# Performance work log

Hardware: AMD Instinct MI355X
Metric: run time of the kernel (lower is better)

## Reference

```python
import jax, jax.numpy as jnp
import numpy as np

L, B, T, C, H, V = 12, 4, 1024, 768, 12, 50257
D = C // H
SCALE = 1.0 / float(np.sqrt(D))
EPS = 1e-5


def layernorm(x, g, b):
    m = jnp.mean(x, axis=-1, keepdims=True)
    v = jnp.var(x, axis=-1, keepdims=True)
    return (x - m) / jnp.sqrt(v + EPS) * g + b


def setup_inputs() -> dict:
    key = jax.random.key(0)
    ks = jax.random.split(key, 12)
    w = lambda k, shape: jax.random.normal(k, shape, jnp.float32) * 0.02
    return {
        "idx": jax.random.randint(ks[0], (B, T), 0, V),
        "tok_emb": w(ks[1], (V, C)),
        "pos_emb": w(ks[2], (1, T, C)),
        # per-layer stacked params (leading dim L); Linear stored [in, out]
        "wq": w(ks[3], (L, C, C)), "bq": jnp.zeros((L, C)),
        "wk": w(ks[4], (L, C, C)), "bk": jnp.zeros((L, C)),
        "wv": w(ks[5], (L, C, C)), "bv": jnp.zeros((L, C)),
        "wo": w(ks[6], (L, C, C)), "bo": jnp.zeros((L, C)),
        "ln1_g": jnp.ones((L, C)), "ln1_b": jnp.zeros((L, C)),
        "ln2_g": jnp.ones((L, C)), "ln2_b": jnp.zeros((L, C)),
        "w1": w(ks[7], (L, C, 4 * C)), "b1": jnp.zeros((L, 4 * C)),
        "w2": w(ks[8], (L, 4 * C, C)), "b2": jnp.zeros((L, C)),
        "lnf_g": jnp.ones((C,)), "lnf_b": jnp.zeros((C,)),
        "head_w": w(ks[9], (C, V)),
    }


def gpt_forward(idx, tok_emb, pos_emb, wq, bq, wk, bk, wv, bv, wo, bo,
                ln1_g, ln1_b, ln2_g, ln2_b, w1, b1, w2, b2,
                lnf_g, lnf_b, head_w):
    t = idx.shape[1]
    x = tok_emb[idx] + pos_emb[:, :t, :]                     # [B,T,C]
    mask = jnp.tril(jnp.ones((t, t), dtype=bool))            # causal

    def block(x, p):
        (pwq, pbq, pwk, pbk, pwv, pbv, pwo, pbo,
         g1, be1, g2, be2, pw1, pb1, pw2, pb2) = p
        h = layernorm(x, g1, be1)
        q = (h @ pwq + pbq).reshape(B, t, H, D)
        k = (h @ pwk + pbk).reshape(B, t, H, D)
        v = (h @ pwv + pbv).reshape(B, t, H, D)
        att = jnp.einsum('bthd,bshd->bhts', q, k) * SCALE    # [B,H,T,T]
        att = jnp.where(mask, att, -jnp.inf)
        att = jax.nn.softmax(att, axis=-1)
        y = jnp.einsum('bhts,bshd->bthd', att, v).reshape(B, t, C)
        x = x + y @ pwo + pbo
        h = layernorm(x, g2, be2)
        x = x + jax.nn.gelu(h @ pw1 + pb1, approximate=False) @ pw2 + pb2
        return x, None

    x, _ = jax.lax.scan(block, x, (wq, bq, wk, bk, wv, bv, wo, bo,
                                   ln1_g, ln1_b, ln2_g, ln2_b,
                                   w1, b1, w2, b2))
    x = layernorm(x, lnf_g, lnf_b)
    return x @ head_w                                        # logits [B,T,V]


def reference(idx, tok_emb, pos_emb, wq, bq, wk, bk, wv, bv, wo, bo,
              ln1_g, ln1_b, ln2_g, ln2_b, w1, b1, w2, b2,
              lnf_g, lnf_b, head_w):
    return gpt_forward(idx, tok_emb, pos_emb, wq, bq, wk, bk, wv, bv, wo, bo,
                       ln1_g, ln1_b, ln2_g, ln2_b, w1, b1, w2, b2,
                       lnf_g, lnf_b, head_w)
```

## Files before the change

### kernel.cpp

```cpp
#include <hip/hip_runtime.h>
#include <hip/hip_bf16.h>
#include <math.h>

#define L_ 12
#define B_ 4
#define T_ 1024
#define C_ 768
#define H_ 12
#define D_ 64
#define V_ 50257
#define M_ 4096
#define QKVN 2304
#define FF_ 3072
#define VPAD_ 50432

typedef __hip_bfloat16 bf16;
typedef __attribute__((ext_vector_type(4))) float f32x4;
typedef __attribute__((ext_vector_type(8))) short short8;
typedef __attribute__((ext_vector_type(8))) __bf16 bf16x8;

typedef __attribute__((address_space(1))) void gvoid;
typedef __attribute__((address_space(3))) void svoid;

__device__ __forceinline__ f32x4 mfma_bf16(short8 a, short8 b, f32x4 c) {
  return __builtin_amdgcn_mfma_f32_16x16x32_bf16(
      __builtin_bit_cast(bf16x8, a), __builtin_bit_cast(bf16x8, b), c, 0, 0, 0);
}

__device__ __forceinline__ void gload_lds16(const void* g, void* l) {
  __builtin_amdgcn_global_load_lds((gvoid*)(void*)g, (svoid*)l, 16, 0, 0);
}

__device__ __forceinline__ short f2bf(float x) {
  return __builtin_bit_cast(short, __float2bfloat16(x));
}

__global__ __launch_bounds__(256) void embed_kernel(const int* __restrict__ idx,
    const float* __restrict__ tok, const float* __restrict__ pos, float* __restrict__ x)
{
  const int row = blockIdx.x;
  const int t = row & (T_ - 1);
  const int id = idx[row];
  const float* te = tok + (size_t)id * C_;
  const float* pe = pos + (size_t)t * C_;
  float* xr = x + (size_t)row * C_;
  const int tid = threadIdx.x;
  xr[tid]       = te[tid]       + pe[tid];
  xr[tid + 256] = te[tid + 256] + pe[tid + 256];
  xr[tid + 512] = te[tid + 512] + pe[tid + 512];
}

__global__ __launch_bounds__(256) void ln_kernel(const float* __restrict__ x,
    const float* __restrict__ g, const float* __restrict__ be, bf16* __restrict__ out)
{
  const int row = blockIdx.x;
  const int tid = threadIdx.x;
  const float* xr = x + (size_t)row * C_;
  float v0 = xr[tid], v1 = xr[tid + 256], v2 = xr[tid + 512];
  float s = v0 + v1 + v2;
  float ss = v0 * v0 + v1 * v1 + v2 * v2;
#pragma unroll
  for (int o = 32; o >= 1; o >>= 1) { s += __shfl_xor(s, o, 64); ss += __shfl_xor(ss, o, 64); }
  __shared__ float sm[8];
  const int w = tid >> 6;
  if ((tid & 63) == 0) { sm[w] = s; sm[4 + w] = ss; }
  __syncthreads();
  s = sm[0] + sm[1] + sm[2] + sm[3];
  ss = sm[4] + sm[5] + sm[6] + sm[7];
  const float mean = s * (1.0f / C_);
  const float var = ss * (1.0f / C_) - mean * mean;
  const float rstd = rsqrtf(var + 1e-5f);
  bf16* orow = out + (size_t)row * C_;
  orow[tid]       = __float2bfloat16((v0 - mean) * rstd * g[tid]       + be[tid]);
  orow[tid + 256] = __float2bfloat16((v1 - mean) * rstd * g[tid + 256] + be[tid + 256]);
  orow[tid + 512] = __float2bfloat16((v2 - mean) * rstd * g[tid + 512] + be[tid + 512]);
}

__global__ __launch_bounds__(256) void convt_kernel(const float* __restrict__ in,
    bf16* __restrict__ out, int K, int N, long in_ls, long out_ls, int row_off)
{
  __shared__ float tile[64][65];
  in  += (size_t)blockIdx.z * in_ls;
  out += (size_t)blockIdx.z * out_ls;
  const int k0 = blockIdx.x * 64, n0 = blockIdx.y * 64;
  const int tid = threadIdx.x;
#pragma unroll
  for (int ph = 0; ph < 16; ph++) {
    int e = ph * 256 + tid;
    int lk = e >> 6, ln = e & 63;
    int gn = n0 + ln;
    tile[lk][ln] = (gn < N) ? in[(size_t)(k0 + lk) * N + gn] : 0.0f;
  }
  __syncthreads();
#pragma unroll
  for (int ph = 0; ph < 16; ph++) {
    int e = ph * 256 + tid;
    int lon = e >> 6, lok = e & 63;
    out[(size_t)(row_off + n0 + lon) * K + k0 + lok] = __float2bfloat16(tile[lok][lon]);
  }
}

__global__ __launch_bounds__(256) void packb_kernel(const float* __restrict__ bq,
    const float* __restrict__ bk, const float* __restrict__ bv, float* __restrict__ out)
{
  const int i = blockIdx.x * 256 + threadIdx.x;
  const int ly = i / QKVN, c = i % QKVN;
  float v;
  if (c < C_)            v = bq[ly * C_ + c];
  else if (c < 2 * C_)   v = bk[ly * C_ + c - C_];
  else                   v = bv[ly * C_ + c - 2 * C_];
  out[i] = v;
}

template<bool BIAS, bool GELU, bool RESID, bool BF16OUT>
__global__ __launch_bounds__(256) void gemm_bt(
    const short* __restrict__ A, const short* __restrict__ Bt,
    const float* __restrict__ bias, const float* resid,
    void* out, int M, int N, int K)
{
  __shared__ short As[128 * 64];
  __shared__ short Bs[128 * 64];
  const int tid = threadIdx.x;
  const int w = tid >> 6, l = tid & 63;
  const int l15 = l & 15, l4 = l >> 4;
  const int wr = w >> 1, wc = w & 1;
  const int nwg = gridDim.x * gridDim.y;
  const int id = blockIdx.y * gridDim.x + blockIdx.x;
  const int chunk = nwg >> 3;
  const int swz = (id & 7) * chunk + (id >> 3);
  const long m0 = (long)(swz % gridDim.x) * 128;
  const long n0 = (long)(swz / gridDim.x) * 128;

  f32x4 acc[4][4] = {};
  const int lrow8 = l >> 3;
  const int lc = l & 7;

  for (int kt = 0; kt < K; kt += 64) {
#pragma unroll
    for (int j = 0; j < 8; j++) {
      const int c = w * 8 + j;
      const int isA = (c < 16);
      const int cc = isA ? c : (c - 16);
      const int row = cc * 8 + lrow8;
      const int colsw = ((lc ^ (row & 7)) << 3);
      const short* gp = (isA ? A + (size_t)(m0 + row) * K : Bt + (size_t)(n0 + row) * K) + kt + colsw;
      short* sp = (isA ? As : Bs) + row * 64 + (lc << 3);
      gload_lds16(gp, sp);
    }
    __syncthreads();
#pragma unroll
    for (int ks = 0; ks < 2; ks++) {
      short8 af[4], bfr[4];
#pragma unroll
      for (int i = 0; i < 4; i++) {
        int row = wr * 64 + i * 16 + l15;
        int cs = (ks * 32 + l4 * 8) ^ ((row & 7) << 3);
        af[i] = *(const short8*)&As[row * 64 + cs];
      }
#pragma unroll
      for (int jn = 0; jn < 4; jn++) {
        int row = wc * 64 + jn * 16 + l15;
        int cs = (ks * 32 + l4 * 8) ^ ((row & 7) << 3);
        bfr[jn] = *(const short8*)&Bs[row * 64 + cs];
      }
#pragma unroll
      for (int i = 0; i < 4; i++)
#pragma unroll
        for (int jn = 0; jn < 4; jn++)
          acc[i][jn] = mfma_bf16(af[i], bfr[jn], acc[i][jn]);
    }
    __syncthreads();
  }

#pragma unroll
  for (int i = 0; i < 4; i++) {
    const long rbase = m0 + wr * 64 + i * 16 + l4 * 4;
#pragma unroll
    for (int jn = 0; jn < 4; jn++) {
      const long col = n0 + wc * 64 + jn * 16 + l15;
      const float bv = BIAS ? bias[col] : 0.0f;
#pragma unroll
      for (int r = 0; r < 4; r++) {
        float v = acc[i][jn][r] + bv;
        if (GELU) v = 0.5f * v * (1.0f + erff(v * 0.70710678118654752f));
        const size_t o = (size_t)(rbase + r) * (size_t)N + col;
        if (RESID)        ((float*)out)[o] = resid[o] + v;
        else if (BF16OUT) ((bf16*)out)[o] = __float2bfloat16(v);
        else              ((float*)out)[o] = v;
      }
    }
  }
}

template<bool BIAS, bool GELU, bool BF16OUT, bool BOUND>
__global__ __launch_bounds__(512, 1) void gemm256(
    const short* __restrict__ A, const short* __restrict__ Bt,
    const float* __restrict__ bias, void* out, int Mb, int N, int K)
{
  __shared__ short As[2][256 * 64];
  __shared__ short Bs[2][256 * 64];
  const int tid = threadIdx.x;
  const int l = tid & 63, l15 = l & 15, l4 = l >> 4;
  const int wv = tid >> 6, wm = wv >> 2, wn = wv & 3;
  const int nwg = gridDim.x, chunkx = nwg >> 3, bid = blockIdx.x;
  const int swz = (bid & 7) * chunkx + (bid >> 3);
  const long m0 = (long)(swz % Mb) * 256;
  const long n0 = (long)(swz / Mb) * 256;
  const int nkt = K >> 6;
  const int rr = tid >> 3, g = tid & 7;

  f32x4 acc[8][4] = {};

  auto stA = [&](int s, int kt, int off) {
#pragma unroll
    for (int p = 0; p < 2; p++) {
      const int r = p * 128 + off + rr;
      gload_lds16(A + (size_t)(m0 + r) * K + (kt << 6) + ((g ^ (r & 7)) << 3),
                  &As[s][r * 64 + g * 8]);
    }
  };
  auto stB = [&](int s, int kt, int off) {
#pragma unroll
    for (int p = 0; p < 2; p++) {
      const int r = p * 128 + ((rr >> 5) << 6) + (rr & 31) + off;
      gload_lds16(Bt + (size_t)(n0 + r) * K + (kt << 6) + ((g ^ (r & 7)) << 3),
                  &Bs[s][r * 64 + g * 8]);
    }
  };
  auto rdA = [&](int s, int mf, int ks) {
    const int row = wm * 128 + mf * 16 + l15;
    const int cs = (ks * 32 + l4 * 8) ^ ((row & 7) << 3);
    return *(const short8*)&As[s][row * 64 + cs];
  };
  auto rdB = [&](int s, int nf, int ks) {
    const int row = wn * 64 + nf * 16 + l15;
    const int cs = (ks * 32 + l4 * 8) ^ ((row & 7) << 3);
    return *(const short8*)&Bs[s][row * 64 + cs];
  };

  stA(0, 0, 0); stB(0, 0, 0); stA(0, 0, 64); stB(0, 0, 32);

  int q = 0;
  for (int kt = 0; kt < nkt; ++kt, q ^= 1) {
    const int ktn = (kt + 1 < nkt) ? kt + 1 : kt;
    short8 a0[2][4], a1[2][4], b0[2][2], b1[2][2];

    stA(q ^ 1, ktn, 0);
    asm volatile("s_waitcnt vmcnt(6)" ::: "memory");
    __builtin_amdgcn_s_barrier();
#pragma unroll
    for (int ks = 0; ks < 2; ks++) {
#pragma unroll
      for (int f = 0; f < 4; f++) a0[ks][f] = rdA(q, f, ks);
#pragma unroll
      for (int j = 0; j < 2; j++) b0[ks][j] = rdB(q, j, ks);
    }
    __builtin_amdgcn_s_setprio(1);
#pragma unroll
    for (int f = 0; f < 4; f++)
#pragma unroll
      for (int j = 0; j < 2; j++) {
        acc[f][j] = mfma_bf16(a0[0][f], b0[0][j], acc[f][j]);
        acc[f][j] = mfma_bf16(a0[1][f], b0[1][j], acc[f][j]);
      }
    __builtin_amdgcn_s_setprio(0);

    stB(q ^ 1, ktn, 0);
    asm volatile("s_waitcnt vmcnt(6)" ::: "memory");
    __builtin_amdgcn_s_barrier();
#pragma unroll
    for (int ks = 0; ks < 2; ks++)
#pragma unroll
      for (int f = 0; f < 4; f++) a1[ks][f] = rdA(q, f + 4, ks);
    __builtin_amdgcn_s_setprio(1);
#pragma unroll
    for (int f = 0; f < 4; f++)
#pragma unroll
      for (int j = 0; j < 2; j++) {
        acc[f + 4][j] = mfma_bf16(a1[0][f], b0[0][j], acc[f + 4][j]);
        acc[f + 4][j] = mfma_bf16(a1[1][f], b0[1][j], acc[f + 4][j]);
      }
    __builtin_amdgcn_s_setprio(0);

    stA(q ^ 1, ktn, 64);
    asm volatile("s_waitcnt vmcnt(6)" ::: "memory");
    __builtin_amdgcn_s_barrier();
#pragma unroll
    for (int ks = 0; ks < 2; ks++)
#pragma unroll
      for (int j = 0; j < 2; j++) b1[ks][j] = rdB(q, j + 2, ks);
    __builtin_amdgcn_s_setprio(1);
#pragma unroll
    for (int f = 0; f < 4; f++)
#pragma unroll
      for (int j = 0; j < 2; j++) {
        acc[f][j + 2] = mfma_bf16(a0[0][f], b1[0][j], acc[f][j + 2]);
        acc[f][j + 2] = mfma_bf16(a0[1][f], b1[1][j], acc[f][j + 2]);
      }
    __builtin_amdgcn_s_setprio(0);

    stB(q ^ 1, ktn, 32);
    __builtin_amdgcn_s_setprio(1);
#pragma unroll
    for (int f = 0; f < 4; f++)
#pragma unroll
      for (int j = 0; j < 2; j++) {
        acc[f + 4][j + 2] = mfma_bf16(a1[0][f], b1[0][j], acc[f + 4][j + 2]);
        acc[f + 4][j + 2] = mfma_bf16(a1[1][f], b1[1][j], acc[f + 4][j + 2]);
      }
    __builtin_amdgcn_s_setprio(0);
  }

#pragma unroll
  for (int i = 0; i < 8; i++) {
#pragma unroll
    for (int j = 0; j < 4; j++) {
      const long col = n0 + wn * 64 + j * 16 + l15;
      if (BOUND && col >= N) continue;
      const float bv = BIAS ? bias[col] : 0.0f;
#pragma unroll
      for (int r = 0; r < 4; r++) {
        const long row = m0 + wm * 128 + i * 16 + l4 * 4 + r;
        float v = acc[i][j][r] + bv;
        if (GELU) v = 0.5f * v * (1.0f + erff(v * 0.70710678118654752f));
        if (BF16OUT) ((bf16*)out)[(size_t)row * (size_t)N + col] = __float2bfloat16(v);
        else         ((float*)out)[(size_t)row * (size_t)N + col] = v;
      }
    }
  }
}

__global__ __launch_bounds__(256) void transv_kernel(const short* __restrict__ qkv,
                                                     short* __restrict__ vt)
{
  __shared__ short tile[64][72];
  const int t0 = blockIdx.x * 64, bh = blockIdx.y;
  const int b = bh / H_, h = bh % H_;
  const int tid = threadIdx.x;
#pragma unroll
  for (int ph = 0; ph < 2; ph++) {
    int lt = ph * 32 + (tid >> 3);
    int ld = (tid & 7) * 8;
    short8 v = *(const short8*)&qkv[(size_t)(b * T_ + t0 + lt) * QKVN + 2 * C_ + h * D_ + ld];
#pragma unroll
    for (int j = 0; j < 8; j++) tile[lt][ld + j] = v[j];
  }
  __syncthreads();
#pragma unroll
  for (int ph = 0; ph < 2; ph++) {
    int ldd = ph * 32 + (tid >> 3);
    int ltt = (tid & 7) * 8;
    short8 v;
#pragma unroll
    for (int j = 0; j < 8; j++) v[j] = tile[ltt + j][ldd];
    *(short8*)&vt[((size_t)bh * D_ + ldd) * T_ + t0 + ltt] = v;
  }
}

__global__ __launch_bounds__(256) void attn_kernel(const short* __restrict__ qkv,
    const short* __restrict__ vt, bf16* __restrict__ y)
{
  __shared__ short Ks[2][64 * 64];
  __shared__ short Vs[2][64 * 64];
  const int qt = (gridDim.x - 1) - blockIdx.x;
  const int bh = blockIdx.y;
  const int b = bh / H_, h = bh % H_;
  const int tid = threadIdx.x, w = tid >> 6, l = tid & 63;
  const int l15 = l & 15, l4 = l >> 4;
  const int qrow0 = qt * 64 + w * 16;
  const float SC2 = 0.125f * 1.44269504088896f;

  auto stageKV = [&](int s, int s0) {
    const short* kbase = qkv + (size_t)(b * T_ + s0) * QKVN + C_ + h * D_;
    const short* vsrc = vt + (size_t)bh * D_ * T_ + s0;
#pragma unroll
    for (int ph = 0; ph < 2; ph++) {
      int r = ph * 32 + (tid >> 3);
      int gk = ((tid & 7) ^ ((r & 3) | (((r >> 3) & 1) << 2))) << 3;
      int gv = ((tid & 7) ^ (r & 7)) << 3;
      gload_lds16(kbase + (size_t)r * QKVN + gk, &Ks[s][r * 64 + (tid & 7) * 8]);
      gload_lds16(vsrc + (size_t)r * T_ + gv, &Vs[s][r * 64 + (tid & 7) * 8]);
    }
  };

  short8 qf[2];
#pragma unroll
  for (int kf = 0; kf < 2; kf++)
    qf[kf] = *(const short8*)&qkv[(size_t)(b * T_ + qrow0 + l15) * QKVN + h * D_ + kf * 32 + l4 * 8];

  f32x4 O[4] = {};
  float mst = -1e30f, lst = 0.0f;

  stageKV(0, 0);
  __syncthreads();

  int cur = 0;
  const int qg = qrow0 + l15;
  const int send = qt * 64 + 64;
  for (int s0 = 0; s0 < send; s0 += 64) {
    if (s0 + 64 < send) stageKV(cur ^ 1, s0 + 64);
    f32x4 S[4];
#pragma unroll
    for (int c = 0; c < 4; c++) {
      const int row = 8 * (l15 >> 2) + (l15 & 3) + 4 * (c & 1) + 32 * (c >> 1);
      const int swz = (row & 3) | (((row >> 3) & 1) << 2);
      short8 k0 = *(const short8*)&Ks[cur][row * 64 + ((l4 ^ swz) << 3)];
      short8 k1 = *(const short8*)&Ks[cur][row * 64 + (((4 + l4) ^ swz) << 3)];
      f32x4 z = {0.0f, 0.0f, 0.0f, 0.0f};
      z = mfma_bf16(k0, qf[0], z);
      z = mfma_bf16(k1, qf[1], z);
      S[c] = z;
    }
#pragma unroll
    for (int c = 0; c < 4; c++) {
      const int kvb = s0 + 8 * l4 + 4 * (c & 1) + 32 * (c >> 1);
#pragma unroll
      for (int r = 0; r < 4; r++) {
        const float v = S[c][r] * SC2;
        S[c][r] = (kvb + r <= qg) ? v : -1e30f;
      }
    }
    float pm = -1e30f;
#pragma unroll
    for (int c = 0; c < 4; c++)
#pragma unroll
      for (int r = 0; r < 4; r++) pm = fmaxf(pm, S[c][r]);
    float mn;
    if (__all(pm - mst <= 8.0f)) {
      mn = mst;
    } else {
      float pm2 = fmaxf(pm, __shfl_xor(pm, 16, 64));
      pm2 = fmaxf(pm2, __shfl_xor(pm2, 32, 64));
      mn = fmaxf(mst, pm2);
      const float al = exp2f(mst - mn);
      mst = mn;
      lst *= al;
#pragma unroll
      for (int r = 0; r < 4; r++) {
        const float alr = __shfl(al, l4 * 4 + r, 16);
#pragma unroll
        for (int df = 0; df < 4; df++) O[df][r] *= alr;
      }
    }
    float rs = 0.0f;
    float pvv[4][4];
#pragma unroll
    for (int c = 0; c < 4; c++)
#pragma unroll
      for (int r = 0; r < 4; r++) { pvv[c][r] = exp2f(S[c][r] - mn); rs += pvv[c][r]; }
    rs += __shfl_xor(rs, 16, 64);
    rs += __shfl_xor(rs, 32, 64);
    lst += rs;
    short8 pa[2];
#pragma unroll
    for (int ks = 0; ks < 2; ks++)
#pragma unroll
      for (int r = 0; r < 4; r++) {
        pa[ks][r]     = f2bf(pvv[2 * ks][r]);
        pa[ks][r + 4] = f2bf(pvv[2 * ks + 1][r]);
      }
#pragma unroll
    for (int df = 0; df < 4; df++) {
      const int row = df * 16 + l15;
      short8 v0 = *(const short8*)&Vs[cur][row * 64 + ((l4 ^ (row & 7)) << 3)];
      short8 v1 = *(const short8*)&Vs[cur][row * 64 + ((((4 + l4)) ^ (row & 7)) << 3)];
      O[df] = mfma_bf16(pa[0], v0, O[df]);
      O[df] = mfma_bf16(pa[1], v1, O[df]);
    }
    __syncthreads();
    cur ^= 1;
  }

  const float inv = 1.0f / lst;
#pragma unroll
  for (int r = 0; r < 4; r++) {
    const float invr = __shfl(inv, l4 * 4 + r, 16);
    const size_t row = (size_t)(b * T_ + qrow0 + l4 * 4 + r);
#pragma unroll
    for (int df = 0; df < 4; df++)
      y[row * C_ + h * D_ + df * 16 + l15] = __float2bfloat16(O[df][r] * invr);
  }
}

extern "C" void kernel_launch(void* const* d_in, const int* in_sizes, int n_in,
                              void* d_out, int out_size, void* d_ws, size_t ws_size,
                              hipStream_t stream)
{
  const int*   idx  = (const int*)d_in[0];
  const float* tok  = (const float*)d_in[1];
  const float* pos  = (const float*)d_in[2];
  const float* wq   = (const float*)d_in[3];
  const float* bq   = (const float*)d_in[4];
  const float* wk   = (const float*)d_in[5];
  const float* bk   = (const float*)d_in[6];
  const float* wv   = (const float*)d_in[7];
  const float* bv   = (const float*)d_in[8];
  const float* wo   = (const float*)d_in[9];
  const float* bo   = (const float*)d_in[10];
  const float* ln1g = (const float*)d_in[11];
  const float* ln1b = (const float*)d_in[12];
  const float* ln2g = (const float*)d_in[13];
  const float* ln2b = (const float*)d_in[14];
  const float* w1   = (const float*)d_in[15];
  const float* b1   = (const float*)d_in[16];
  const float* w2   = (const float*)d_in[17];
  const float* b2   = (const float*)d_in[18];
  const float* lnfg = (const float*)d_in[19];
  const float* lnfb = (const float*)d_in[20];
  const float* headw= (const float*)d_in[21];

  char* p = (char*)d_ws;
  size_t off = 0;
  auto alloc = [&](size_t n) { void* r = p + off; off += (n + 255) & ~(size_t)255; return r; };
  short* qkvT  = (short*)alloc((size_t)L_ * QKVN * C_ * 2);
  short* woT   = (short*)alloc((size_t)L_ * C_ * C_ * 2);
  short* w1T   = (short*)alloc((size_t)L_ * FF_ * C_ * 2);
  short* w2T   = (short*)alloc((size_t)L_ * C_ * FF_ * 2);
  short* headT = (short*)alloc((size_t)VPAD_ * C_ * 2);
  float* qkvb  = (float*)alloc((size_t)L_ * QKVN * 4);
  float* x     = (float*)alloc((size_t)M_ * C_ * 4);
  bf16*  h     = (bf16*)alloc((size_t)M_ * C_ * 2);
  short* qkvB  = (short*)alloc((size_t)M_ * QKVN * 2);
  short* vt    = (short*)alloc((size_t)B_ * H_ * D_ * T_ * 2);
  short* y     = (short*)alloc((size_t)M_ * C_ * 2);
  short* hid   = (short*)alloc((size_t)M_ * FF_ * 2);
  if (off > ws_size) return;

  convt_kernel<<<dim3(12, 12, 12), 256, 0, stream>>>(wq, (bf16*)qkvT, C_, C_, (long)C_ * C_, (long)QKVN * C_, 0);
  convt_kernel<<<dim3(12, 12, 12), 256, 0, stream>>>(wk, (bf16*)qkvT, C_, C_, (long)C_ * C_, (long)QKVN * C_, C_);
  convt_kernel<<<dim3(12, 12, 12), 256, 0, stream>>>(wv, (bf16*)qkvT, C_, C_, (long)C_ * C_, (long)QKVN * C_, 2 * C_);
  convt_kernel<<<dim3(12, 12, 12), 256, 0, stream>>>(wo, (bf16*)woT, C_, C_, (long)C_ * C_, (long)C_ * C_, 0);
  convt_kernel<<<dim3(12, 48, 12), 256, 0, stream>>>(w1, (bf16*)w1T, C_, FF_, (long)C_ * FF_, (long)FF_ * C_, 0);
  convt_kernel<<<dim3(48, 12, 12), 256, 0, stream>>>(w2, (bf16*)w2T, FF_, C_, (long)FF_ * C_, (long)C_ * FF_, 0);
  convt_kernel<<<dim3(12, VPAD_ / 64, 1), 256, 0, stream>>>(headw, (bf16*)headT, C_, V_, 0, 0, 0);
  packb_kernel<<<dim3(108), 256, 0, stream>>>(bq, bk, bv, qkvb);

  embed_kernel<<<dim3(M_), 256, 0, stream>>>(idx, tok, pos, x);

  for (int ly = 0; ly < L_; ly++) {
    ln_kernel<<<dim3(M_), 256, 0, stream>>>(x, ln1g + ly * C_, ln1b + ly * C_, h);
    gemm_bt<true, false, false, true><<<dim3(32, 18), 256, 0, stream>>>(
        (const short*)h, qkvT + (size_t)ly * QKVN * C_, qkvb + ly * QKVN, nullptr, qkvB, M_, QKVN, C_);
    transv_kernel<<<dim3(16, 48), 256, 0, stream>>>(qkvB, vt);
    attn_kernel<<<dim3(16, 48), 256, 0, stream>>>(qkvB, vt, (bf16*)y);
    gemm_bt<true, false, true, false><<<dim3(32, 6), 256, 0, stream>>>(
        y, woT + (size_t)ly * C_ * C_, bo + ly * C_, x, x, M_, C_, C_);
    ln_kernel<<<dim3(M_), 256, 0, stream>>>(x, ln2g + ly * C_, ln2b + ly * C_, h);
    gemm_bt<true, true, false, true><<<dim3(32, 24), 256, 0, stream>>>(
        (const short*)h, w1T + (size_t)ly * FF_ * C_, b1 + ly * FF_, nullptr, hid, M_, FF_, C_);
    gemm_bt<true, false, true, false><<<dim3(32, 6), 256, 0, stream>>>(
        hid, w2T + (size_t)ly * C_ * FF_, b2 + ly * C_, x, x, M_, C_, FF_);
  }

  ln_kernel<<<dim3(M_), 256, 0, stream>>>(x, lnfg, lnfb, h);
  gemm256<false, false, false, true><<<dim3((M_ / 256) * (VPAD_ / 256)), 512, 0, stream>>>(
      (const short*)h, headT, nullptr, d_out, M_ / 256, V_, C_);
}
```

Before: 3.513 ms.

## Double-buffer layer GEMM LDS staging and remap head GEMM tiles for cache locality

The per-layer 128x128 GEMM now uses two LDS buffers: the next K-tile is prefetched with global_load_lds while MFMAs run on the current one, synchronised by explicit vmcnt waits and barriers instead of two __syncthreads per iteration. It also asks for two workgroups per CU. The LM-head GEMM drops its unused template options and replaces the generic swizzle with a fixed tile mapping over a 16x200 grid, using a vocab pad of 51200, so that the eight groups of blocks cover distinct M/N regions for better L2/MALL reuse. The risks are doubled LDS use (64KB per block), which may limit occupancy, and extra padded head-weight tiles plus a hardcoded grid mapping.

```diff
diff --git a/kernel.cpp b/kernel.cpp
--- a/kernel.cpp
+++ b/kernel.cpp
@@ -12,7 +12,7 @@
 #define M_ 4096
 #define QKVN 2304
 #define FF_ 3072
-#define VPAD_ 50432
+#define VPAD_ 51200
 
 typedef __hip_bfloat16 bf16;
 typedef __attribute__((ext_vector_type(4))) float f32x4;
@@ -113,13 +113,13 @@
 }
 
 template<bool BIAS, bool GELU, bool RESID, bool BF16OUT>
-__global__ __launch_bounds__(256) void gemm_bt(
+__global__ __launch_bounds__(256, 2) void gemm_bt(
     const short* __restrict__ A, const short* __restrict__ Bt,
     const float* __restrict__ bias, const float* resid,
     void* out, int M, int N, int K)
 {
-  __shared__ short As[128 * 64];
-  __shared__ short Bs[128 * 64];
+  __shared__ short As[2][128 * 64];
+  __shared__ short Bs[2][128 * 64];
   const int tid = threadIdx.x;
   const int w = tid >> 6, l = tid & 63;
   const int l15 = l & 15, l4 = l >> 4;
@@ -130,24 +130,31 @@
   const int swz = (id & 7) * chunk + (id >> 3);
   const long m0 = (long)(swz % gridDim.x) * 128;
   const long n0 = (long)(swz / gridDim.x) * 128;
+  const int nkt = K >> 6;
+  const int rr = tid >> 3, g = tid & 7;
 
   f32x4 acc[4][4] = {};
-  const int lrow8 = l >> 3;
-  const int lc = l & 7;
-
-  for (int kt = 0; kt < K; kt += 64) {
-#pragma unroll
-    for (int j = 0; j < 8; j++) {
-      const int c = w * 8 + j;
-      const int isA = (c < 16);
-      const int cc = isA ? c : (c - 16);
-      const int row = cc * 8 + lrow8;
-      const int colsw = ((lc ^ (row & 7)) << 3);
-      const short* gp = (isA ? A + (size_t)(m0 + row) * K : Bt + (size_t)(n0 + row) * K) + kt + colsw;
-      short* sp = (isA ? As : Bs) + row * 64 + (lc << 3);
-      gload_lds16(gp, sp);
-    }
-    __syncthreads();
+
+  auto stage = [&](int s, int kt) {
+#pragma unroll
+    for (int p = 0; p < 4; p++) {
+      const int row = p * 32 + rr;
+      const int cg = ((g ^ (row & 7)) << 3);
+      gload_lds16(A  + (size_t)(m0 + row) * K + (kt << 6) + cg, &As[s][row * 64 + g * 8]);
+      gload_lds16(Bt + (size_t)(n0 + row) * K + (kt << 6) + cg, &Bs[s][row * 64 + g * 8]);
+    }
+  };
+
+  stage(0, 0);
+  int buf = 0;
+  for (int kt = 0; kt < nkt; ++kt) {
+    if (kt + 1 < nkt) {
+      stage(buf ^ 1, kt + 1);
+      asm volatile("s_waitcnt vmcnt(8)" ::: "memory");
+    } else {
+      asm volatile("s_waitcnt vmcnt(0)" ::: "memory");
+    }
+    __builtin_amdgcn_s_barrier();
 #pragma unroll
     for (int ks = 0; ks < 2; ks++) {
       short8 af[4], bfr[4];
@@ -155,13 +162,13 @@
       for (int i = 0; i < 4; i++) {
         int row = wr * 64 + i * 16 + l15;
         int cs = (ks * 32 + l4 * 8) ^ ((row & 7) << 3);
-        af[i] = *(const short8*)&As[row * 64 + cs];
+        af[i] = *(const short8*)&As[buf][row * 64 + cs];
       }
 #pragma unroll
       for (int jn = 0; jn < 4; jn++) {
         int row = wc * 64 + jn * 16 + l15;
         int cs = (ks * 32 + l4 * 8) ^ ((row & 7) << 3);
-        bfr[jn] = *(const short8*)&Bs[row * 64 + cs];
+        bfr[jn] = *(const short8*)&Bs[buf][row * 64 + cs];
       }
 #pragma unroll
       for (int i = 0; i < 4; i++)
@@ -169,7 +176,8 @@
         for (int jn = 0; jn < 4; jn++)
           acc[i][jn] = mfma_bf16(af[i], bfr[jn], acc[i][jn]);
     }
-    __syncthreads();
+    __builtin_amdgcn_s_barrier();
+    buf ^= 1;
   }
 
 #pragma unroll
@@ -192,20 +200,21 @@
   }
 }
 
-template<bool BIAS, bool GELU, bool BF16OUT, bool BOUND>
 __global__ __launch_bounds__(512, 1) void gemm256(
     const short* __restrict__ A, const short* __restrict__ Bt,
-    const float* __restrict__ bias, void* out, int Mb, int N, int K)
+    float* __restrict__ out, int N, int K)
 {
   __shared__ short As[2][256 * 64];
   __shared__ short Bs[2][256 * 64];
   const int tid = threadIdx.x;
   const int l = tid & 63, l15 = l & 15, l4 = l >> 4;
   const int wv = tid >> 6, wm = wv >> 2, wn = wv & 3;
-  const int nwg = gridDim.x, chunkx = nwg >> 3, bid = blockIdx.x;
-  const int swz = (bid & 7) * chunkx + (bid >> 3);
-  const long m0 = (long)(swz % Mb) * 256;
-  const long n0 = (long)(swz / Mb) * 256;
+  const int bid = blockIdx.x;
+  const int x = bid & 7, r = bid >> 3;
+  const int mt = (x & 1) * 8 + (r & 7);
+  const int nt = (x >> 1) * 50 + (r >> 3);
+  const long m0 = (long)mt * 256;
+  const long n0 = (long)nt * 256;
   const int nkt = K >> 6;
   const int rr = tid >> 3, g = tid & 7;
 
@@ -214,17 +223,17 @@
   auto stA = [&](int s, int kt, int off) {
 #pragma unroll
     for (int p = 0; p < 2; p++) {
-      const int r = p * 128 + off + rr;
-      gload_lds16(A + (size_t)(m0 + r) * K + (kt << 6) + ((g ^ (r & 7)) << 3),
-                  &As[s][r * 64 + g * 8]);
+      const int row = p * 128 + off + rr;
+      gload_lds16(A + (size_t)(m0 + row) * K + (kt << 6) + ((g ^ (row & 7)) << 3),
+                  &As[s][row * 64 + g * 8]);
     }
   };
   auto stB = [&](int s, int kt, int off) {
 #pragma unroll
     for (int p = 0; p < 2; p++) {
-      const int r = p * 128 + ((rr >> 5) << 6) + (rr & 31) + off;
-      gload_lds16(Bt + (size_t)(n0 + r) * K + (kt << 6) + ((g ^ (r & 7)) << 3),
-                  &Bs[s][r * 64 + g * 8]);
+      const int row = p * 128 + ((rr >> 5) << 6) + (rr & 31) + off;
+      gload_lds16(Bt + (size_t)(n0 + row) * K + (kt << 6) + ((g ^ (row & 7)) << 3),
+                  &Bs[s][row * 64 + g * 8]);
     }
   };
   auto rdA = [&](int s, int mf, int ks) {
@@ -316,15 +325,11 @@
 #pragma unroll
     for (int j = 0; j < 4; j++) {
       const long col = n0 + wn * 64 + j * 16 + l15;
-      if (BOUND && col >= N) continue;
-      const float bv = BIAS ? bias[col] : 0.0f;
+      if (col >= N) continue;
 #pragma unroll
       for (int r = 0; r < 4; r++) {
         const long row = m0 + wm * 128 + i * 16 + l4 * 4 + r;
-        float v = acc[i][j][r] + bv;
-        if (GELU) v = 0.5f * v * (1.0f + erff(v * 0.70710678118654752f));
-        if (BF16OUT) ((bf16*)out)[(size_t)row * (size_t)N + col] = __float2bfloat16(v);
-        else         ((float*)out)[(size_t)row * (size_t)N + col] = v;
+        out[(size_t)row * (size_t)N + col] = acc[i][j][r];
       }
     }
   }
@@ -553,6 +558,5 @@
   }
 
   ln_kernel<<<dim3(M_), 256, 0, stream>>>(x, lnfg, lnfb, h);
-  gemm256<false, false, false, true><<<dim3((M_ / 256) * (VPAD_ / 256)), 512, 0, stream>>>(
-      (const short*)h, headT, nullptr, d_out, M_ / 256, V_, C_);
-}
+  gemm256<<<dim3(3200), 512, 0, stream>>>((const short*)h, headT, (float*)d_out, V_, C_);
+}
```

After: 3.708 ms. +5.6%, slower.

## Remap LM-head GEMM tiles per XCD and use nontemporal output stores

Applied to the files above, without the earlier changes.

The LM-head GEMM grid is padded from 197 to 200 column tiles so it has 3200 workgroups. Each group of 8 consecutive block IDs is split so that each XCD works on a block of 8 row tiles by 50 column tiles, which improves L2 reuse of A and B within an XCD. Output logits and the transposed V buffer are now written with nontemporal stores to avoid polluting cache. The padded columns add extra compute (about 1.5%), and the headT weight buffer must be allocated up to the new VPAD_ or the extra tiles will read out of bounds.

```diff
diff --git a/kernel.cpp b/kernel.cpp
--- a/kernel.cpp
+++ b/kernel.cpp
@@ -12,7 +12,7 @@
 #define M_ 4096
 #define QKVN 2304
 #define FF_ 3072
-#define VPAD_ 50432
+#define VPAD_ 51200
 
 typedef __hip_bfloat16 bf16;
 typedef __attribute__((ext_vector_type(4))) float f32x4;
@@ -192,20 +192,21 @@
   }
 }
 
-template<bool BIAS, bool GELU, bool BF16OUT, bool BOUND>
 __global__ __launch_bounds__(512, 1) void gemm256(
     const short* __restrict__ A, const short* __restrict__ Bt,
-    const float* __restrict__ bias, void* out, int Mb, int N, int K)
+    float* __restrict__ out, int N, int K)
 {
   __shared__ short As[2][256 * 64];
   __shared__ short Bs[2][256 * 64];
   const int tid = threadIdx.x;
   const int l = tid & 63, l15 = l & 15, l4 = l >> 4;
   const int wv = tid >> 6, wm = wv >> 2, wn = wv & 3;
-  const int nwg = gridDim.x, chunkx = nwg >> 3, bid = blockIdx.x;
-  const int swz = (bid & 7) * chunkx + (bid >> 3);
-  const long m0 = (long)(swz % Mb) * 256;
-  const long n0 = (long)(swz / Mb) * 256;
+  const int bid = blockIdx.x;
+  const int x = bid & 7, r = bid >> 3;
+  const int mt = (x & 1) * 8 + (r & 7);
+  const int nt = (x >> 1) * 50 + (r >> 3);
+  const long m0 = (long)mt * 256;
+  const long n0 = (long)nt * 256;
   const int nkt = K >> 6;
   const int rr = tid >> 3, g = tid & 7;
 
@@ -214,17 +215,17 @@
   auto stA = [&](int s, int kt, int off) {
 #pragma unroll
     for (int p = 0; p < 2; p++) {
-      const int r = p * 128 + off + rr;
-      gload_lds16(A + (size_t)(m0 + r) * K + (kt << 6) + ((g ^ (r & 7)) << 3),
-                  &As[s][r * 64 + g * 8]);
+      const int row = p * 128 + off + rr;
+      gload_lds16(A + (size_t)(m0 + row) * K + (kt << 6) + ((g ^ (row & 7)) << 3),
+                  &As[s][row * 64 + g * 8]);
     }
   };
   auto stB = [&](int s, int kt, int off) {
 #pragma unroll
     for (int p = 0; p < 2; p++) {
-      const int r = p * 128 + ((rr >> 5) << 6) + (rr & 31) + off;
-      gload_lds16(Bt + (size_t)(n0 + r) * K + (kt << 6) + ((g ^ (r & 7)) << 3),
-                  &Bs[s][r * 64 + g * 8]);
+      const int row = p * 128 + ((rr >> 5) << 6) + (rr & 31) + off;
+      gload_lds16(Bt + (size_t)(n0 + row) * K + (kt << 6) + ((g ^ (row & 7)) << 3),
+                  &Bs[s][row * 64 + g * 8]);
     }
   };
   auto rdA = [&](int s, int mf, int ks) {
@@ -316,15 +317,11 @@
 #pragma unroll
     for (int j = 0; j < 4; j++) {
       const long col = n0 + wn * 64 + j * 16 + l15;
-      if (BOUND && col >= N) continue;
-      const float bv = BIAS ? bias[col] : 0.0f;
+      if (col >= N) continue;
 #pragma unroll
       for (int r = 0; r < 4; r++) {
         const long row = m0 + wm * 128 + i * 16 + l4 * 4 + r;
-        float v = acc[i][j][r] + bv;
-        if (GELU) v = 0.5f * v * (1.0f + erff(v * 0.70710678118654752f));
-        if (BF16OUT) ((bf16*)out)[(size_t)row * (size_t)N + col] = __float2bfloat16(v);
-        else         ((float*)out)[(size_t)row * (size_t)N + col] = v;
+        __builtin_nontemporal_store(acc[i][j][r], &out[(size_t)row * (size_t)N + col]);
       }
     }
   }
@@ -353,7 +350,7 @@
     short8 v;
 #pragma unroll
     for (int j = 0; j < 8; j++) v[j] = tile[ltt + j][ldd];
-    *(short8*)&vt[((size_t)bh * D_ + ldd) * T_ + t0 + ltt] = v;
+    __builtin_nontemporal_store(v, (short8*)&vt[((size_t)bh * D_ + ldd) * T_ + t0 + ltt]);
   }
 }
 
@@ -553,6 +550,5 @@
   }
 
   ln_kernel<<<dim3(M_), 256, 0, stream>>>(x, lnfg, lnfb, h);
-  gemm256<false, false, false, true><<<dim3((M_ / 256) * (VPAD_ / 256)), 512, 0, stream>>>(
-      (const short*)h, headT, nullptr, d_out, M_ / 256, V_, C_);
-}
+  gemm256<<<dim3(3200), 512, 0, stream>>>((const short*)h, headT, (float*)d_out, V_, C_);
+}
```

New measurement: 3.847 ms. +9.5%, slower.
